# Optimization experiments

Hardware: AMD Instinct MI355X
Metric: run time of the kernel (lower is better)

## Reference

```python
import jax, jax.numpy as jnp
import numpy as np

# Key insight: 'take the first candidate in descending-score order that is not yet
# used' is exactly 'argmax of the score over unused items'. Since vocab == 25 and
# every index has a char, the Python fallback branch is unreachable for
# seq_len <= vocab. So the whole greedy dedup collapses to a masked-argmax scan
# over positions, vectorized across the batch.

def setup_inputs() -> dict:
    key = jax.random.key(0)
    B, S, V = 65536, 25, 25
    matrix = jax.random.normal(key, (B, S, V), dtype=jnp.float32)
    return {"matrix": matrix}


def reference(matrix):
    B, S, V = matrix.shape
    neg = jnp.finfo(matrix.dtype).min

    def step(used, scores):  # used: [B,V] bool, scores: [B,V]
        masked = jnp.where(used, neg, scores)
        sel = jnp.argmax(masked, axis=-1)                       # [B] greedy pick
        val = jnp.take_along_axis(scores, sel[:, None], axis=-1)[:, 0]
        used = used | jax.nn.one_hot(sel, V, dtype=bool)        # mark as used
        return used, (sel, val)

    used0 = jnp.zeros((B, V), dtype=bool)
    _, (sels, vals) = jax.lax.scan(step, used0, jnp.swapaxes(matrix, 0, 1))
    # actions: [B,S] int32 item ids (== char index, char = chr(id + ord('A')))
    actions = jnp.swapaxes(sels, 0, 1).astype(jnp.int32)
    sel_scores = jnp.swapaxes(vals, 0, 1)                        # [B,S] float
    return actions, sel_scores
```

## Files before the change

### kernel.cpp

```cpp
#include <hip/hip_runtime.h>
#include <float.h>


#define S_LEN 25
#define VOCAB 25
#define ROWS 16
#define THREADS 64
#define ROW_DW (S_LEN * VOCAB)
#define BLK_DW (ROWS * ROW_DW)
#define OUT_DW (ROWS * S_LEN)
#define DMA_FULL (BLK_DW / 256)
#define TAIL_DW (BLK_DW - DMA_FULL * 256)

__device__ __forceinline__ void gld16(const float* g, float* l) {
  __builtin_amdgcn_global_load_lds(
      (const __attribute__((address_space(1))) void*)g,
      (__attribute__((address_space(3))) void*)l, 16, 0, 0);
}

__global__ __launch_bounds__(THREADS) void greedy_dedup_kernel(
    const float* __restrict__ m, float* __restrict__ out, int B) {
  __shared__ __align__(16) float buf[BLK_DW];

  const int t = threadIdx.x;
  const long long blk = blockIdx.x;
  const float* src = m + blk * (long long)BLK_DW;

#pragma unroll
  for (int k = 0; k < DMA_FULL; ++k)
    gld16(src + k * 256 + t * 4, &buf[k * 256]);
  if (t < TAIL_DW)
    buf[DMA_FULL * 256 + t] = src[DMA_FULL * 256 + t];
  __syncthreads();

  const int row = t & 15;
  const int h = t >> 4;
  const int vb = h * 6;
  const float* myrow = &buf[row * ROW_DW];

  unsigned used = 0u;
  float acts[S_LEN], vals[S_LEN];
  float cur[7], nxt[7];
#pragma unroll
  for (int j = 0; j < 7; ++j) cur[j] = myrow[vb + j];

#pragma unroll
  for (int s = 0; s < S_LEN; ++s) {
    if (s + 1 < S_LEN) {
#pragma unroll
      for (int j = 0; j < 7; ++j) nxt[j] = myrow[(s + 1) * VOCAB + vb + j];
    }

    float best = -FLT_MAX;
    int bi = 31;
#pragma unroll
    for (int j = 0; j < 7; ++j) {
      int vv = vb + j;
      bool fr = ((used >> vv) & 1u) == 0u;
      if (fr && cur[j] > best) { best = cur[j]; bi = vv; }
    }

    float ob = __shfl_xor(best, 16); int oi = __shfl_xor(bi, 16);
    if (ob > best || (ob == best && oi < bi)) { best = ob; bi = oi; }
    ob = __shfl_xor(best, 32); oi = __shfl_xor(bi, 32);
    if (ob > best || (ob == best && oi < bi)) { best = ob; bi = oi; }

    used |= (1u << bi);
    acts[s] = (float)bi;
    vals[s] = best;

#pragma unroll
    for (int j = 0; j < 7; ++j) cur[j] = nxt[j];
  }

  if (h == 0) {
#pragma unroll
    for (int s = 0; s < S_LEN; ++s) {
      buf[row * S_LEN + s] = acts[s];
      buf[OUT_DW + row * S_LEN + s] = vals[s];
    }
  }
  __syncthreads();

  float* gact = out + blk * OUT_DW;
  float* gval = out + (long long)B * S_LEN + blk * OUT_DW;
#pragma unroll
  for (int k = 0; k < 7; ++k) {
    int idx = k * 64 + t;
    if (idx < OUT_DW) {
      gact[idx] = buf[idx];
      gval[idx] = buf[OUT_DW + idx];
    }
  }
}

extern "C" void kernel_launch(void* const* d_in, const int* in_sizes, int n_in,
                              void* d_out, int out_size, void* d_ws, size_t ws_size,
                              hipStream_t stream) {
  const float* m = (const float*)d_in[0];
  float* out = (float*)d_out;
  int B = in_sizes[0] / ROW_DW;
  int grid = B / ROWS;
  greedy_dedup_kernel<<<grid, THREADS, 0, stream>>>(m, out, B);
}
```

Measured before the change: 259.4 us.

## Halve rows per block, widen per-row lanes, stage loads through registers

Each block now handles 8 rows instead of 16, so the grid doubles and each block uses half the LDS. Each row is split across 8 lanes with overlapping 4-wide vocab windows, and a third xor-shuffle step completes the argmax reduction. The global_load_lds DMA path is replaced by a register-staged float4 prefetch ring that copies data into LDS. The goal is more blocks in flight to hide memory latency, at the cost of one extra shuffle per serial step and explicit register copies.

Result: faster. 248.0 us (-4.4%).

```diff
diff --git a/kernel.cpp b/kernel.cpp
--- a/kernel.cpp
+++ b/kernel.cpp
@@ -4,19 +4,15 @@
 
 #define S_LEN 25
 #define VOCAB 25
-#define ROWS 16
+#define ROWS 8
 #define THREADS 64
 #define ROW_DW (S_LEN * VOCAB)
 #define BLK_DW (ROWS * ROW_DW)
+#define BLK_V4 (BLK_DW / 4)
+#define FULL_ROUNDS (BLK_V4 / 64)
+#define TAIL_V4 (BLK_V4 - FULL_ROUNDS * 64)
 #define OUT_DW (ROWS * S_LEN)
-#define DMA_FULL (BLK_DW / 256)
-#define TAIL_DW (BLK_DW - DMA_FULL * 256)
-
-__device__ __forceinline__ void gld16(const float* g, float* l) {
-  __builtin_amdgcn_global_load_lds(
-      (const __attribute__((address_space(1))) void*)g,
-      (__attribute__((address_space(3))) void*)l, 16, 0, 0);
-}
+#define DEPTH 8
 
 __global__ __launch_bounds__(THREADS) void greedy_dedup_kernel(
     const float* __restrict__ m, float* __restrict__ out, int B) {
@@ -24,53 +20,62 @@
 
   const int t = threadIdx.x;
   const long long blk = blockIdx.x;
-  const float* src = m + blk * (long long)BLK_DW;
+  const float4* src4 = (const float4*)(m + blk * (long long)BLK_DW);
+  float4* buf4 = (float4*)buf;
 
+  float4 reg[DEPTH];
 #pragma unroll
-  for (int k = 0; k < DMA_FULL; ++k)
-    gld16(src + k * 256 + t * 4, &buf[k * 256]);
-  if (t < TAIL_DW)
-    buf[DMA_FULL * 256 + t] = src[DMA_FULL * 256 + t];
+  for (int k = 0; k < DEPTH; ++k) reg[k] = src4[k * 64 + t];
+#pragma unroll
+  for (int k = 0; k < FULL_ROUNDS; ++k) {
+    float4 v = reg[k & (DEPTH - 1)];
+    if (k + DEPTH < FULL_ROUNDS)
+      reg[k & (DEPTH - 1)] = src4[(k + DEPTH) * 64 + t];
+    buf4[k * 64 + t] = v;
+  }
+  if (t < TAIL_V4) buf4[FULL_ROUNDS * 64 + t] = src4[FULL_ROUNDS * 64 + t];
   __syncthreads();
 
-  const int row = t & 15;
-  const int h = t >> 4;
-  const int vb = h * 6;
+  const int row = t & 7;
+  const int h = t >> 3;
+  const int vb = h * 3;
   const float* myrow = &buf[row * ROW_DW];
 
   unsigned used = 0u;
   float acts[S_LEN], vals[S_LEN];
-  float cur[7], nxt[7];
+  float cur[4], nxt[4];
 #pragma unroll
-  for (int j = 0; j < 7; ++j) cur[j] = myrow[vb + j];
+  for (int j = 0; j < 4; ++j) cur[j] = myrow[vb + j];
 
 #pragma unroll
   for (int s = 0; s < S_LEN; ++s) {
     if (s + 1 < S_LEN) {
 #pragma unroll
-      for (int j = 0; j < 7; ++j) nxt[j] = myrow[(s + 1) * VOCAB + vb + j];
+      for (int j = 0; j < 4; ++j) nxt[j] = myrow[(s + 1) * VOCAB + vb + j];
     }
 
     float best = -FLT_MAX;
     int bi = 31;
 #pragma unroll
-    for (int j = 0; j < 7; ++j) {
+    for (int j = 0; j < 4; ++j) {
       int vv = vb + j;
       bool fr = ((used >> vv) & 1u) == 0u;
       if (fr && cur[j] > best) { best = cur[j]; bi = vv; }
     }
 
-    float ob = __shfl_xor(best, 16); int oi = __shfl_xor(bi, 16);
-    if (ob > best || (ob == best && oi < bi)) { best = ob; bi = oi; }
-    ob = __shfl_xor(best, 32); oi = __shfl_xor(bi, 32);
-    if (ob > best || (ob == best && oi < bi)) { best = ob; bi = oi; }
+#pragma unroll
+    for (int d = 8; d <= 32; d <<= 1) {
+      float ob = __shfl_xor(best, d);
+      int oi = __shfl_xor(bi, d);
+      if (ob > best || (ob == best && oi < bi)) { best = ob; bi = oi; }
+    }
 
     used |= (1u << bi);
     acts[s] = (float)bi;
     vals[s] = best;
 
 #pragma unroll
-    for (int j = 0; j < 7; ++j) cur[j] = nxt[j];
+    for (int j = 0; j < 4; ++j) cur[j] = nxt[j];
   }
 
   if (h == 0) {
@@ -85,7 +90,7 @@
   float* gact = out + blk * OUT_DW;
   float* gval = out + (long long)B * S_LEN + blk * OUT_DW;
 #pragma unroll
-  for (int k = 0; k < 7; ++k) {
+  for (int k = 0; k < 4; ++k) {
     int idx = k * 64 + t;
     if (idx < OUT_DW) {
       gact[idx] = buf[idx];
```
